# Performance work log

Hardware: AMD Instinct MI355X
Metric: run time of the kernel (lower is better)

Reference implementation:

```python
import jax, jax.numpy as jnp
import numpy as np

N_NODES = 8192
N_EDGES = 262144
IN_F, HID, OUT_F = 512, 512, 256


def setup_inputs() -> dict:
    key = jax.random.key(0)
    k_x, k_e, k_w1, k_b1, k_w2, k_b2 = jax.random.split(key, 6)
    x = jax.random.normal(k_x, (N_NODES, IN_F), dtype=jnp.float32)
    edge_index = jax.random.randint(k_e, (2, N_EDGES), 0, N_NODES, dtype=jnp.int64)
    # xavier-uniform linear weights, stored as [in, out]
    def xavier(k, fan_in, fan_out):
        lim = np.sqrt(6.0 / (fan_in + fan_out)).astype(np.float32)
        return jax.random.uniform(k, (fan_in, fan_out), jnp.float32, -lim, lim)
    W1 = xavier(k_w1, IN_F, HID)
    b1 = jax.random.uniform(k_b1, (HID,), jnp.float32, -0.05, 0.05)
    W2 = xavier(k_w2, HID, OUT_F)
    b2 = jax.random.uniform(k_b2, (OUT_F,), jnp.float32, -0.05, 0.05)
    return {"x": x, "edge_index": edge_index, "W1": W1, "b1": b1, "W2": W2, "b2": b2}


def _gcn_layer(x, edge_index, W, b):
    # H' = D~^{-1/2} A~ D~^{-1/2} H W + b, with A~ = A + I
    n = x.shape[0]
    adj = jnp.zeros((n, n), dtype=x.dtype).at[edge_index[0], edge_index[1]].set(1.0)
    adj = adj + jnp.eye(n, dtype=x.dtype)
    degree = jnp.clip(adj.sum(axis=1), 1.0, None)
    d_inv_sqrt = degree ** -0.5
    adj_norm = adj * d_inv_sqrt[None, :] * d_inv_sqrt[:, None]
    return (adj_norm @ x) @ W + b


def reference(x, edge_index, W1, b1, W2, b2):
    h = jax.nn.relu(_gcn_layer(x, edge_index, W1, b1))
    # dropout p=0.0 -> identity
    out = _gcn_layer(h, edge_index, W2, b2)
    return out
```

## Files before the change

### kernel.cpp

```cpp
#include <hip/hip_runtime.h>
#include <hip/hip_bf16.h>
#include <stdint.h>

#define N_NODES 8192
#define N_EDGES 262144
#define IN_F 512
#define HID 512
#define OUT_F 256
#define CAP 128

typedef __attribute__((ext_vector_type(8))) short short8;
typedef __attribute__((ext_vector_type(4))) float f32x4;

__device__ __forceinline__ float bflo(unsigned int u) {
  union { unsigned int x; float f; } c; c.x = u << 16; return c.f;
}
__device__ __forceinline__ float bfhi(unsigned int u) {
  union { unsigned int x; float f; } c; c.x = u & 0xffff0000u; return c.f;
}
__device__ __forceinline__ unsigned short f2bf(float f) {
  union { float f; unsigned int u; } c; c.f = f;
  unsigned int r = c.u + 0x7fffu + ((c.u >> 16) & 1u);
  return (unsigned short)(r >> 16);
}

__device__ __forceinline__ void gload_lds16(const void* g, void* l) {
  __builtin_amdgcn_global_load_lds((const __attribute__((address_space(1))) void*)g,
                                   (__attribute__((address_space(3))) void*)l, 16, 0, 0);
}

#define NB_CVT  4096
#define NB_W1T  64
#define NB_W2T  32
#define NB_EDGE 1024

__device__ __forceinline__ void transpose_tile64(
    const float* __restrict__ W, unsigned short* __restrict__ Wt,
    int K, int N, int kb, int nb, int tid, float (*tile)[65]) {
  const int k0g = kb * 64, n0g = nb * 64;
  const int r = tid >> 4;
  const int c4 = (tid & 15) * 4;
#pragma unroll
  for (int rr = 0; rr < 4; ++rr) {
    const int k = rr * 16 + r;
    const float4 v = *(const float4*)&W[(size_t)(k0g + k) * N + n0g + c4];
    tile[k][c4] = v.x; tile[k][c4 + 1] = v.y; tile[k][c4 + 2] = v.z; tile[k][c4 + 3] = v.w;
  }
  __syncthreads();
  const int n = tid >> 2;
  const int kq = (tid & 3) * 16;
  unsigned int o[8];
#pragma unroll
  for (int q = 0; q < 8; ++q) {
    unsigned int lo = f2bf(tile[kq + 2 * q][n]);
    unsigned int hi = f2bf(tile[kq + 2 * q + 1][n]);
    o[q] = lo | (hi << 16);
  }
  unsigned int* dst = (unsigned int*)&Wt[(size_t)(n0g + n) * K + k0g + kq];
  *(uint4*)dst       = make_uint4(o[0], o[1], o[2], o[3]);
  *(uint4*)(dst + 4) = make_uint4(o[4], o[5], o[6], o[7]);
}

__global__ __launch_bounds__(256) void prep_all(
    const float* __restrict__ x, const float* __restrict__ W1, const float* __restrict__ W2,
    const int* __restrict__ ei,
    unsigned short* __restrict__ Xb, unsigned short* __restrict__ W1t,
    unsigned short* __restrict__ W2t, int* __restrict__ cnt, int* __restrict__ adj) {
  __shared__ float tile[64][65];
  const int b = blockIdx.x, tid = threadIdx.x;
  if (b < NB_CVT) {
    int idx = b * 256 + tid;
    const float4 v = ((const float4*)x)[idx];
    uint2 o;
    o.x = (unsigned int)f2bf(v.x) | ((unsigned int)f2bf(v.y) << 16);
    o.y = (unsigned int)f2bf(v.z) | ((unsigned int)f2bf(v.w) << 16);
    ((uint2*)Xb)[idx] = o;
  } else if (b < NB_CVT + NB_W1T) {
    int t = b - NB_CVT;
    transpose_tile64(W1, W1t, IN_F, HID, t >> 3, t & 7, tid, tile);
  } else if (b < NB_CVT + NB_W1T + NB_W2T) {
    int t = b - NB_CVT - NB_W1T;
    transpose_tile64(W2, W2t, HID, OUT_F, t >> 2, t & 3, tid, tile);
  } else {
    int e = (b - NB_CVT - NB_W1T - NB_W2T) * 256 + tid;
    int i = ei[e];
    int j = ei[N_EDGES + e];
    int p = atomicAdd(&cnt[i], 1);
    if (p < CAP) adj[i * CAP + p] = j;
  }
}

__global__ __launch_bounds__(128) void dedup_node(
    int* __restrict__ cnt, int* __restrict__ adj, float* __restrict__ dis) {
  const int i = blockIdx.x, t = threadIdx.x;
  __shared__ int js[CAP];
  __shared__ unsigned char keep[CAP];
  int n0 = cnt[i]; if (n0 > CAP) n0 = CAP;
  if (t < n0) js[t] = adj[i * CAP + t];
  __syncthreads();
  bool k = false;
  if (t < n0) {
    k = true;
    int jt = js[t];
    for (int s = 0; s < t; ++s) if (js[s] == jt) { k = false; break; }
  }
  keep[t] = k;
  __syncthreads();
  if (k) {
    int r = 0;
    for (int s = 0; s < t; ++s) r += keep[s];
    adj[i * CAP + r] = js[t];
  }
  if (t == 0) {
    int nd = 0;
    for (int s = 0; s < n0; ++s) nd += keep[s];
    cnt[i] = nd;
    dis[i] = rsqrtf((float)(nd + 1));
  }
}

template<int BM, int BN>
__global__ __launch_bounds__(256) void gemm_bt(
    const unsigned short* __restrict__ A, const unsigned short* __restrict__ Bt,
    unsigned short* __restrict__ C, int M, int N, int K) {
  constexpr int MR = BM / 32, NR = BN / 32;
  __shared__ __align__(16) unsigned short As[BM * 64];
  __shared__ __align__(16) unsigned short Bs[BN * 64];
  const int tid = threadIdx.x;
  const long row0 = (long)blockIdx.x * BM;
  const long col0 = (long)blockIdx.y * BN;
  const int lane = tid & 63;
  const int wid = tid >> 6;
  const int ln15 = lane & 15, hi = lane >> 4;
  const int wr = (wid >> 1) * (BM / 2), wc = (wid & 1) * (BN / 2);
  const int sr = tid >> 3;
  const int sk = (tid & 7) * 8;
  f32x4 acc[MR][NR] = {};

  for (int k0 = 0; k0 < K; k0 += 64) {
#pragma unroll
    for (int c = 0; c < MR; ++c)
      gload_lds16(A  + (row0 + c * 32 + sr) * (long)K + k0 + sk, &As[(c * 256 + tid) * 8]);
#pragma unroll
    for (int c = 0; c < NR; ++c)
      gload_lds16(Bt + (col0 + c * 32 + sr) * (long)K + k0 + sk, &Bs[(c * 256 + tid) * 8]);
    __syncthreads();
#pragma unroll
    for (int kk = 0; kk < 64; kk += 32) {
      short8 a[MR], b[NR];
#pragma unroll
      for (int m = 0; m < MR; ++m)
        a[m] = *(const short8*)&As[(wr + m * 16 + ln15) * 64 + kk + hi * 8];
#pragma unroll
      for (int n = 0; n < NR; ++n)
        b[n] = *(const short8*)&Bs[(wc + n * 16 + ln15) * 64 + kk + hi * 8];
#pragma unroll
      for (int m = 0; m < MR; ++m)
#pragma unroll
        for (int n = 0; n < NR; ++n)
          acc[m][n] = __builtin_amdgcn_mfma_f32_16x16x32_bf16(a[m], b[n], acc[m][n], 0, 0, 0);
    }
    __syncthreads();
  }
#pragma unroll
  for (int m = 0; m < MR; ++m)
#pragma unroll
    for (int n = 0; n < NR; ++n)
#pragma unroll
      for (int r = 0; r < 4; ++r) {
        long row = row0 + wr + m * 16 + hi * 4 + r;
        long col = col0 + wc + n * 16 + ln15;
        C[row * N + col] = f2bf(acc[m][n][r]);
      }
}

__global__ __launch_bounds__(256) void aggregate_relu(
    const unsigned short* __restrict__ T, const int* __restrict__ cnt,
    const int* __restrict__ adj, const float* __restrict__ dis,
    const float* __restrict__ bias, unsigned short* __restrict__ H) {
  const int w = threadIdx.x >> 6, lane = threadIdx.x & 63;
  const int i = blockIdx.x * 4 + w;
  __shared__ uint2 jw[4][CAP];
  const int n = cnt[i];
  for (int e0 = 0; e0 < n; e0 += 64)
    if (e0 + lane < n) {
      int j = adj[i * CAP + e0 + lane];
      jw[w][e0 + lane] = make_uint2((unsigned int)j, __float_as_uint(dis[j]));
    }
  __syncthreads();
  float a[8] = {};
  const float di = dis[i];
  int e = 0;
  for (; e + 2 <= n; e += 2) {
    const uint2 p0 = jw[w][e], p1 = jw[w][e + 1];
    const uint4 v0 = *(const uint4*)&T[(size_t)p0.x * 512 + lane * 8];
    const uint4 v1 = *(const uint4*)&T[(size_t)p1.x * 512 + lane * 8];
    const float w0 = __uint_as_float(p0.y), w1 = __uint_as_float(p1.y);
    a[0] += w0 * bflo(v0.x); a[1] += w0 * bfhi(v0.x);
    a[2] += w0 * bflo(v0.y); a[3] += w0 * bfhi(v0.y);
    a[4] += w0 * bflo(v0.z); a[5] += w0 * bfhi(v0.z);
    a[6] += w0 * bflo(v0.w); a[7] += w0 * bfhi(v0.w);
    a[0] += w1 * bflo(v1.x); a[1] += w1 * bfhi(v1.x);
    a[2] += w1 * bflo(v1.y); a[3] += w1 * bfhi(v1.y);
    a[4] += w1 * bflo(v1.z); a[5] += w1 * bfhi(v1.z);
    a[6] += w1 * bflo(v1.w); a[7] += w1 * bfhi(v1.w);
  }
  if (e < n) {
    const uint2 p0 = jw[w][e];
    const uint4 v0 = *(const uint4*)&T[(size_t)p0.x * 512 + lane * 8];
    const float w0 = __uint_as_float(p0.y);
    a[0] += w0 * bflo(v0.x); a[1] += w0 * bfhi(v0.x);
    a[2] += w0 * bflo(v0.y); a[3] += w0 * bfhi(v0.y);
    a[4] += w0 * bflo(v0.z); a[5] += w0 * bfhi(v0.z);
    a[6] += w0 * bflo(v0.w); a[7] += w0 * bfhi(v0.w);
  }
  {
    const uint4 vs = *(const uint4*)&T[(size_t)i * 512 + lane * 8];
    a[0] += di * bflo(vs.x); a[1] += di * bfhi(vs.x);
    a[2] += di * bflo(vs.y); a[3] += di * bfhi(vs.y);
    a[4] += di * bflo(vs.z); a[5] += di * bfhi(vs.z);
    a[6] += di * bflo(vs.w); a[7] += di * bfhi(vs.w);
  }
  const float4 b0 = *(const float4*)&bias[lane * 8];
  const float4 b1 = *(const float4*)&bias[lane * 8 + 4];
  float h[8];
  h[0] = fmaxf(di * a[0] + b0.x, 0.f); h[1] = fmaxf(di * a[1] + b0.y, 0.f);
  h[2] = fmaxf(di * a[2] + b0.z, 0.f); h[3] = fmaxf(di * a[3] + b0.w, 0.f);
  h[4] = fmaxf(di * a[4] + b1.x, 0.f); h[5] = fmaxf(di * a[5] + b1.y, 0.f);
  h[6] = fmaxf(di * a[6] + b1.z, 0.f); h[7] = fmaxf(di * a[7] + b1.w, 0.f);
  uint4 o;
  o.x = (unsigned int)f2bf(h[0]) | ((unsigned int)f2bf(h[1]) << 16);
  o.y = (unsigned int)f2bf(h[2]) | ((unsigned int)f2bf(h[3]) << 16);
  o.z = (unsigned int)f2bf(h[4]) | ((unsigned int)f2bf(h[5]) << 16);
  o.w = (unsigned int)f2bf(h[6]) | ((unsigned int)f2bf(h[7]) << 16);
  *(uint4*)&H[(size_t)i * 512 + lane * 8] = o;
}

__global__ __launch_bounds__(256) void aggregate_out(
    const unsigned short* __restrict__ T, const int* __restrict__ cnt,
    const int* __restrict__ adj, const float* __restrict__ dis,
    const float* __restrict__ bias, float* __restrict__ out) {
  const int w = threadIdx.x >> 6, lane = threadIdx.x & 63;
  const int i = blockIdx.x * 4 + w;
  __shared__ uint2 jw[4][CAP];
  const int n = cnt[i];
  for (int e0 = 0; e0 < n; e0 += 64)
    if (e0 + lane < n) {
      int j = adj[i * CAP + e0 + lane];
      jw[w][e0 + lane] = make_uint2((unsigned int)j, __float_as_uint(dis[j]));
    }
  __syncthreads();
  float a[4] = {};
  const float di = dis[i];
  int e = 0;
  for (; e + 2 <= n; e += 2) {
    const uint2 p0 = jw[w][e], p1 = jw[w][e + 1];
    const uint2 v0 = *(const uint2*)&T[(size_t)p0.x * 256 + lane * 4];
    const uint2 v1 = *(const uint2*)&T[(size_t)p1.x * 256 + lane * 4];
    const float w0 = __uint_as_float(p0.y), w1 = __uint_as_float(p1.y);
    a[0] += w0 * bflo(v0.x); a[1] += w0 * bfhi(v0.x);
    a[2] += w0 * bflo(v0.y); a[3] += w0 * bfhi(v0.y);
    a[0] += w1 * bflo(v1.x); a[1] += w1 * bfhi(v1.x);
    a[2] += w1 * bflo(v1.y); a[3] += w1 * bfhi(v1.y);
  }
  if (e < n) {
    const uint2 p0 = jw[w][e];
    const uint2 v0 = *(const uint2*)&T[(size_t)p0.x * 256 + lane * 4];
    const float w0 = __uint_as_float(p0.y);
    a[0] += w0 * bflo(v0.x); a[1] += w0 * bfhi(v0.x);
    a[2] += w0 * bflo(v0.y); a[3] += w0 * bfhi(v0.y);
  }
  {
    const uint2 vs = *(const uint2*)&T[(size_t)i * 256 + lane * 4];
    a[0] += di * bflo(vs.x); a[1] += di * bfhi(vs.x);
    a[2] += di * bflo(vs.y); a[3] += di * bfhi(vs.y);
  }
  const float4 bb = *(const float4*)&bias[lane * 4];
  float4 o;
  o.x = di * a[0] + bb.x;
  o.y = di * a[1] + bb.y;
  o.z = di * a[2] + bb.z;
  o.w = di * a[3] + bb.w;
  *(float4*)&out[(size_t)i * 256 + lane * 4] = o;
}

extern "C" void kernel_launch(void* const* d_in, const int* in_sizes, int n_in,
                              void* d_out, int out_size, void* d_ws, size_t ws_size,
                              hipStream_t stream) {
  const float* x  = (const float*)d_in[0];
  const int*   ei = (const int*)d_in[1];
  const float* W1 = (const float*)d_in[2];
  const float* b1 = (const float*)d_in[3];
  const float* W2 = (const float*)d_in[4];
  const float* b2 = (const float*)d_in[5];
  float* out = (float*)d_out;

  char* ws = (char*)d_ws;
  int* cnt   = (int*)ws;                     ws += 32768;
  int* adj   = (int*)ws;                     ws += (size_t)N_NODES * CAP * 4;
  float* dis = (float*)ws;                   ws += 32768;
  unsigned short* Xb  = (unsigned short*)ws; ws += (size_t)N_NODES * IN_F * 2;
  unsigned short* W1t = (unsigned short*)ws; ws += (size_t)IN_F * HID * 2;
  unsigned short* W2t = (unsigned short*)ws; ws += (size_t)HID * OUT_F * 2;
  unsigned short* T1  = (unsigned short*)ws; ws += (size_t)N_NODES * HID * 2;
  unsigned short* H   = (unsigned short*)ws; ws += (size_t)N_NODES * HID * 2;
  unsigned short* T2  = (unsigned short*)ws; ws += (size_t)N_NODES * OUT_F * 2;

  hipMemsetAsync(cnt, 0, 32768, stream);

  prep_all<<<NB_CVT + NB_W1T + NB_W2T + NB_EDGE, 256, 0, stream>>>(
      x, W1, W2, ei, Xb, W1t, W2t, cnt, adj);
  dedup_node<<<N_NODES, 128, 0, stream>>>(cnt, adj, dis);

  gemm_bt<128, 64><<<dim3(N_NODES / 128, HID / 64), 256, 0, stream>>>(Xb, W1t, T1, N_NODES, HID, IN_F);
  aggregate_relu<<<N_NODES / 4, 256, 0, stream>>>(T1, cnt, adj, dis, b1, H);

  gemm_bt<64, 64><<<dim3(N_NODES / 64, OUT_F / 64), 256, 0, stream>>>(H, W2t, T2, N_NODES, OUT_F, HID);
  aggregate_out<<<N_NODES / 4, 256, 0, stream>>>(T2, cnt, adj, dis, b2, out);
}
```

Measured before the change: 162.4 us.

## Deduplicate edges with atomic bitmap in prep, drop dedup kernel

Edge deduplication moves into the edge-scatter stage: a dense N×N bitmap (8 MB) is set with atomicOr, and only first-seen edges are appended to the adjacency list. This removes the separate per-node dedup kernel launch and its quadratic scan. Degree normalisation is now computed on the fly from cnt in the aggregation kernels instead of being stored in a dis array. In exchange, an 8 MB memset is added every call, along with scattered atomics into a large bitmap.

```diff
diff --git a/kernel.cpp b/kernel.cpp
--- a/kernel.cpp
+++ b/kernel.cpp
@@ -65,7 +65,8 @@
     const float* __restrict__ x, const float* __restrict__ W1, const float* __restrict__ W2,
     const int* __restrict__ ei,
     unsigned short* __restrict__ Xb, unsigned short* __restrict__ W1t,
-    unsigned short* __restrict__ W2t, int* __restrict__ cnt, int* __restrict__ adj) {
+    unsigned short* __restrict__ W2t, unsigned int* __restrict__ bitmap,
+    int* __restrict__ cnt, int* __restrict__ adj) {
   __shared__ float tile[64][65];
   const int b = blockIdx.x, tid = threadIdx.x;
   if (b < NB_CVT) {
@@ -85,37 +86,13 @@
     int e = (b - NB_CVT - NB_W1T - NB_W2T) * 256 + tid;
     int i = ei[e];
     int j = ei[N_EDGES + e];
-    int p = atomicAdd(&cnt[i], 1);
-    if (p < CAP) adj[i * CAP + p] = j;
-  }
-}
-
-__global__ __launch_bounds__(128) void dedup_node(
-    int* __restrict__ cnt, int* __restrict__ adj, float* __restrict__ dis) {
-  const int i = blockIdx.x, t = threadIdx.x;
-  __shared__ int js[CAP];
-  __shared__ unsigned char keep[CAP];
-  int n0 = cnt[i]; if (n0 > CAP) n0 = CAP;
-  if (t < n0) js[t] = adj[i * CAP + t];
-  __syncthreads();
-  bool k = false;
-  if (t < n0) {
-    k = true;
-    int jt = js[t];
-    for (int s = 0; s < t; ++s) if (js[s] == jt) { k = false; break; }
-  }
-  keep[t] = k;
-  __syncthreads();
-  if (k) {
-    int r = 0;
-    for (int s = 0; s < t; ++s) r += keep[s];
-    adj[i * CAP + r] = js[t];
-  }
-  if (t == 0) {
-    int nd = 0;
-    for (int s = 0; s < n0; ++s) nd += keep[s];
-    cnt[i] = nd;
-    dis[i] = rsqrtf((float)(nd + 1));
+    int lin = i * N_NODES + j;
+    unsigned int bit = 1u << (lin & 31);
+    unsigned int old = atomicOr(&bitmap[lin >> 5], bit);
+    if (!(old & bit)) {
+      int p = atomicAdd(&cnt[i], 1);
+      if (p < CAP) adj[i * CAP + p] = j;
+    }
   }
 }
 
@@ -176,8 +153,8 @@
 
 __global__ __launch_bounds__(256) void aggregate_relu(
     const unsigned short* __restrict__ T, const int* __restrict__ cnt,
-    const int* __restrict__ adj, const float* __restrict__ dis,
-    const float* __restrict__ bias, unsigned short* __restrict__ H) {
+    const int* __restrict__ adj, const float* __restrict__ bias,
+    unsigned short* __restrict__ H) {
   const int w = threadIdx.x >> 6, lane = threadIdx.x & 63;
   const int i = blockIdx.x * 4 + w;
   __shared__ uint2 jw[4][CAP];
@@ -185,11 +162,12 @@
   for (int e0 = 0; e0 < n; e0 += 64)
     if (e0 + lane < n) {
       int j = adj[i * CAP + e0 + lane];
-      jw[w][e0 + lane] = make_uint2((unsigned int)j, __float_as_uint(dis[j]));
+      float dj = rsqrtf((float)(cnt[j] + 1));
+      jw[w][e0 + lane] = make_uint2((unsigned int)j, __float_as_uint(dj));
     }
   __syncthreads();
   float a[8] = {};
-  const float di = dis[i];
+  const float di = rsqrtf((float)(n + 1));
   int e = 0;
   for (; e + 2 <= n; e += 2) {
     const uint2 p0 = jw[w][e], p1 = jw[w][e + 1];
@@ -238,8 +216,8 @@
 
 __global__ __launch_bounds__(256) void aggregate_out(
     const unsigned short* __restrict__ T, const int* __restrict__ cnt,
-    const int* __restrict__ adj, const float* __restrict__ dis,
-    const float* __restrict__ bias, float* __restrict__ out) {
+    const int* __restrict__ adj, const float* __restrict__ bias,
+    float* __restrict__ out) {
   const int w = threadIdx.x >> 6, lane = threadIdx.x & 63;
   const int i = blockIdx.x * 4 + w;
   __shared__ uint2 jw[4][CAP];
@@ -247,11 +225,12 @@
   for (int e0 = 0; e0 < n; e0 += 64)
     if (e0 + lane < n) {
       int j = adj[i * CAP + e0 + lane];
-      jw[w][e0 + lane] = make_uint2((unsigned int)j, __float_as_uint(dis[j]));
+      float dj = rsqrtf((float)(cnt[j] + 1));
+      jw[w][e0 + lane] = make_uint2((unsigned int)j, __float_as_uint(dj));
     }
   __syncthreads();
   float a[4] = {};
-  const float di = dis[i];
+  const float di = rsqrtf((float)(n + 1));
   int e = 0;
   for (; e + 2 <= n; e += 2) {
     const uint2 p0 = jw[w][e], p1 = jw[w][e + 1];
@@ -296,9 +275,9 @@
   float* out = (float*)d_out;
 
   char* ws = (char*)d_ws;
+  unsigned int* bitmap = (unsigned int*)ws;  ws += 8388608;
   int* cnt   = (int*)ws;                     ws += 32768;
   int* adj   = (int*)ws;                     ws += (size_t)N_NODES * CAP * 4;
-  float* dis = (float*)ws;                   ws += 32768;
   unsigned short* Xb  = (unsigned short*)ws; ws += (size_t)N_NODES * IN_F * 2;
   unsigned short* W1t = (unsigned short*)ws; ws += (size_t)IN_F * HID * 2;
   unsigned short* W2t = (unsigned short*)ws; ws += (size_t)HID * OUT_F * 2;
@@ -306,15 +285,14 @@
   unsigned short* H   = (unsigned short*)ws; ws += (size_t)N_NODES * HID * 2;
   unsigned short* T2  = (unsigned short*)ws; ws += (size_t)N_NODES * OUT_F * 2;
 
-  hipMemsetAsync(cnt, 0, 32768, stream);
+  hipMemsetAsync(bitmap, 0, 8388608 + 32768, stream);
 
   prep_all<<<NB_CVT + NB_W1T + NB_W2T + NB_EDGE, 256, 0, stream>>>(
-      x, W1, W2, ei, Xb, W1t, W2t, cnt, adj);
-  dedup_node<<<N_NODES, 128, 0, stream>>>(cnt, adj, dis);
+      x, W1, W2, ei, Xb, W1t, W2t, bitmap, cnt, adj);
 
   gemm_bt<128, 64><<<dim3(N_NODES / 128, HID / 64), 256, 0, stream>>>(Xb, W1t, T1, N_NODES, HID, IN_F);
-  aggregate_relu<<<N_NODES / 4, 256, 0, stream>>>(T1, cnt, adj, dis, b1, H);
+  aggregate_relu<<<N_NODES / 4, 256, 0, stream>>>(T1, cnt, adj, b1, H);
 
   gemm_bt<64, 64><<<dim3(N_NODES / 64, OUT_F / 64), 256, 0, stream>>>(H, W2t, T2, N_NODES, OUT_F, HID);
-  aggregate_out<<<N_NODES / 4, 256, 0, stream>>>(T2, cnt, adj, dis, b2, out);
-}
+  aggregate_out<<<N_NODES / 4, 256, 0, stream>>>(T2, cnt, adj, b2, out);
+}
```

Result: no change. 160.8 us (-1.0%).
